# Kernel tuning notes

Hardware: AMD Instinct MI355X
Metric: run time of the kernel (lower is better)

Reference implementation:

```python
import jax, jax.numpy as jnp
import numpy as np
import math

T, S, B, E, H = 2048, 2048, 4, 1024, 16
D = E // H


def setup_inputs() -> dict:
    key = jax.random.key(0)
    ks = jax.random.split(key, 12)
    inp = {
        "query": jax.random.normal(ks[0], (T, B, E), jnp.float32),
        "key": jax.random.normal(ks[1], (S, B, E), jnp.float32),
        "value": jax.random.normal(ks[2], (S, B, E), jnp.float32),
        # causal mask: True means masked (matches torch masked_fill semantics)
        "attn_mask": jnp.triu(jnp.ones((T, S), dtype=bool), k=1),
        # torch Linear layout: weight [out_features, in_features]
        "Wq": jax.random.normal(ks[3], (E, E), jnp.float32) * (1.0 / math.sqrt(E)),
        "bq": jax.random.normal(ks[4], (E,), jnp.float32) * 0.02,
        "Wk": jax.random.normal(ks[5], (E, E), jnp.float32) * (1.0 / math.sqrt(E)),
        "bk": jax.random.normal(ks[6], (E,), jnp.float32) * 0.02,
        "Wv": jax.random.normal(ks[7], (E, E), jnp.float32) * (1.0 / math.sqrt(E)),
        "bv": jax.random.normal(ks[8], (E,), jnp.float32) * 0.02,
        "Wo": jax.random.normal(ks[9], (E, E), jnp.float32) * (1.0 / math.sqrt(E)),
        "bo": jax.random.normal(ks[10], (E,), jnp.float32) * 0.02,
    }
    return inp


def reference(query, key, value, attn_mask, Wq, bq, Wk, bk, Wv, bv, Wo, bo):
    # inputs are [T/S, B, E] (batch_first=False); compute in [B, H, T, D]
    q = (jnp.einsum('tbe,fe->btf', query, Wq) + bq).reshape(B, T, H, D).transpose(0, 2, 1, 3)
    k = (jnp.einsum('sbe,fe->bsf', key, Wk) + bk).reshape(B, S, H, D).transpose(0, 2, 1, 3)
    v = (jnp.einsum('sbe,fe->bsf', value, Wv) + bv).reshape(B, S, H, D).transpose(0, 2, 1, 3)

    scores = jnp.einsum('bhtd,bhsd->bhts', q, k) / math.sqrt(D)  # [B,H,T,S]
    masked = jnp.where(attn_mask[None, None, :, :], -jnp.inf, scores)
    # custom numerics: epsilon-shifted softmax, then re-zero -inf positions
    probs = jax.nn.softmax(masked + 1e-9, axis=-1)
    probs = jnp.where(jnp.isinf(masked), 0.0, probs)

    out = jnp.einsum('bhts,bhsd->bhtd', probs, v)  # [B,H,T,D]
    out = out.transpose(0, 2, 1, 3).reshape(B, T, E)
    out = out @ Wo.T + bo
    return out.transpose(1, 0, 2)  # back to [T, B, E]
```

## Files before the change

kernel.cpp:

```cpp
#include <hip/hip_runtime.h>

typedef unsigned short u16;
typedef __attribute__((ext_vector_type(8))) __bf16 bf16x8;
typedef __attribute__((ext_vector_type(4))) float f32x4;
typedef __attribute__((ext_vector_type(16))) float f32x16;
typedef __attribute__((ext_vector_type(4))) unsigned short u16x4;
typedef __attribute__((ext_vector_type(8))) unsigned short u16x8;
typedef __attribute__((ext_vector_type(4))) unsigned int u32x4;

#define T_LEN 2048
#define B_SZ 4
#define E_DIM 1024
#define H_N 16
#define D_H 64
#define M_ROWS (T_LEN * B_SZ)
#define NQT (T_LEN / 128)

__device__ __forceinline__ u16 f2bf(float f){
  unsigned u = __builtin_bit_cast(unsigned, f);
  u += 0x7fffu + ((u >> 16) & 1u);
  return (u16)(u >> 16);
}

__device__ __forceinline__ float fexp2(float x){
#if __has_builtin(__builtin_amdgcn_exp2f)
  return __builtin_amdgcn_exp2f(x);
#else
  return exp2f(x);
#endif
}

__device__ __forceinline__ unsigned cvtpk(float lo, float hi){
  unsigned w;
  asm("v_cvt_pk_bf16_f32 %0, %1, %2" : "=v"(w) : "v"(lo), "v"(hi));
  return w;
}
__device__ __forceinline__ float xhalf_max(float x){
  return fmaxf(x, __shfl_xor(x, 32));
}
__device__ __forceinline__ float xhalf_sum(float x){
  return x + __shfl_xor(x, 32);
}

__device__ __forceinline__ void load_lds16(const void* g, void* l){
  __builtin_amdgcn_global_load_lds(
      (const __attribute__((address_space(1))) void*)g,
      (__attribute__((address_space(3))) void*)l, 16, 0, 0);
}

__global__ void cvt_all(
    const float* __restrict__ i0, const float* __restrict__ i1, const float* __restrict__ i2,
    const float* __restrict__ i3, const float* __restrict__ i4, const float* __restrict__ i5,
    const float* __restrict__ i6,
    u16* __restrict__ o0, u16* __restrict__ o1, u16* __restrict__ o2,
    u16* __restrict__ o3, u16* __restrict__ o4, u16* __restrict__ o5,
    u16* __restrict__ o6, int nX, int nW)
{
  const int z = blockIdx.z;
  const float* in; u16* out; int n;
  switch (z){
    case 0: in=i0; out=o0; n=nX; break;
    case 1: in=i1; out=o1; n=nX; break;
    case 2: in=i2; out=o2; n=nX; break;
    case 3: in=i3; out=o3; n=nW; break;
    case 4: in=i4; out=o4; n=nW; break;
    case 5: in=i5; out=o5; n=nW; break;
    default: in=i6; out=o6; n=nW; break;
  }
  int idx = (blockIdx.x * blockDim.x + threadIdx.x) * 4;
  int stride = gridDim.x * blockDim.x * 4;
  for (int i = idx; i < n; i += stride){
    float4 v = *(const float4*)(in + i);
    u16x4 o = { f2bf(v.x), f2bf(v.y), f2bf(v.z), f2bf(v.w) };
    *(u16x4*)(out + i) = o;
  }
}

#define G4_LDSU16 32768

__device__ __forceinline__ void stageG(const u16* __restrict__ G, int r0g, int k0,
                                       char* base, int buf, int tid){
  #pragma unroll
  for (int r=0;r<2;++r){
    int c = r*256 + tid;
    int row = c >> 2;
    int colb = ((c & 3) * 16) ^ (((row >> 2) & 3) << 4);
    load_lds16((const char*)(G + (size_t)(r0g + row)*E_DIM + k0) + colb,
               base + buf*8192 + (size_t)(r*256 + (tid >> 6)*64)*16);
  }
}

__device__ __forceinline__ void gemm4_mainloop(
    const u16* __restrict__ A, const u16* __restrict__ Bt,
    int m0, int n0, u16* smem, f32x4 (&acc)[4][4])
{
  constexpr int NT = E_DIM / 32;
  const int tid = threadIdx.x;
  const int lane = tid & 63;
  const int w = tid >> 6;
  const int wr = w >> 1, wc = w & 1;
  const int lr = lane & 15, lg = lane >> 4;
  char* Abase = (char*)smem;
  char* Bbase = (char*)smem + 32768;

  #pragma unroll
  for (int i=0;i<4;i++)
    #pragma unroll
    for (int j=0;j<4;j++) acc[i][j] = (f32x4){0.f,0.f,0.f,0.f};

  stageG(A,  m0, 0,  Abase, 0, tid);
  stageG(Bt, n0, 0,  Bbase, 0, tid);
  stageG(A,  m0, 32, Abase, 1, tid);
  stageG(Bt, n0, 32, Bbase, 1, tid);
  asm volatile("s_waitcnt vmcnt(4)\n" ::: "memory");
  __builtin_amdgcn_sched_barrier(0);
  __builtin_amdgcn_s_barrier();

  const int cbx = (lg*16) ^ (((lr >> 2) & 3) << 4);

  for (int t = 0; t < NT; ++t){
    const int buf = t & 3;
    if (t + 2 < NT){
      stageG(A,  m0, (t+2)*32, Abase, (t+2) & 3, tid);
      stageG(Bt, n0, (t+2)*32, Bbase, (t+2) & 3, tid);
    }
    char* Ac = Abase + buf*8192;
    char* Bc = Bbase + buf*8192;
    bf16x8 af[4], bfr[4];
    #pragma unroll
    for (int i=0;i<4;i++){
      af[i]  = *(const bf16x8*)(Ac + (wr*64 + i*16 + lr)*64 + cbx);
      bfr[i] = *(const bf16x8*)(Bc + (wc*64 + i*16 + lr)*64 + cbx);
    }
    asm volatile("s_waitcnt lgkmcnt(0)\n" ::: "memory");
    __builtin_amdgcn_sched_barrier(0);
    __builtin_amdgcn_s_setprio(1);
    #pragma unroll
    for (int i=0;i<4;i++)
      #pragma unroll
      for (int j=0;j<4;j++)
        acc[i][j] = __builtin_amdgcn_mfma_f32_16x16x32_bf16(af[i], bfr[j], acc[i][j], 0,0,0);
    __builtin_amdgcn_s_setprio(0);
    if (t + 2 < NT)      asm volatile("s_waitcnt vmcnt(4)\n" ::: "memory");
    else if (t + 1 < NT) asm volatile("s_waitcnt vmcnt(0)\n" ::: "memory");
    __builtin_amdgcn_sched_barrier(0);
    __builtin_amdgcn_s_barrier();
  }
}

__device__ __forceinline__ void xcd_remap_gemm(int &m0, int &n0){
  int L = blockIdx.y * 8 + blockIdx.x;
  int c = L & 7, i = L >> 3;
  int by = c*8 + (i & 7);
  int bx = i >> 3;
  m0 = by * 128; n0 = bx * 128;
}

struct QKVArgs {
  const u16* A[3]; const u16* Bw[3]; const float* bias[3];
  float scale[3]; u16* out[3];
};

__global__ __launch_bounds__(256) void gemm_qkv(QKVArgs args){
  __shared__ __align__(16) u16 smem[G4_LDSU16];
  const int z = blockIdx.z;
  int m0, n0; xcd_remap_gemm(m0, n0);
  f32x4 acc[4][4];
  gemm4_mainloop(args.A[z], args.Bw[z], m0, n0, smem, acc);

  const int lane = threadIdx.x & 63;
  const int w = threadIdx.x >> 6;
  const int wr = w >> 1, wc = w & 1;
  const int lr = lane & 15, lg = lane >> 4;
  const float* bias = args.bias[z];
  const float scale = args.scale[z];
  u16* outB = args.out[z];
  #pragma unroll
  for (int i=0;i<4;i++)
    #pragma unroll
    for (int j=0;j<4;j++)
      #pragma unroll
      for (int q=0;q<4;q++){
        int m = m0 + wr*64 + i*16 + lg*4 + q;
        int n = n0 + wc*64 + j*16 + lr;
        float v = (acc[i][j][q] + bias[n]) * scale;
        int t = m >> 2, b = m & 3;
        int h = n >> 6, d = n & 63;
        outB[ ((size_t)(b*H_N + h)*T_LEN + t)*D_H + d ] = f2bf(v);
      }
}

__global__ __launch_bounds__(256) void gemm_out(
    const u16* __restrict__ A, const u16* __restrict__ Bt,
    const float* __restrict__ bias, float* __restrict__ outF)
{
  __shared__ __align__(16) u16 smem[G4_LDSU16];
  int m0, n0; xcd_remap_gemm(m0, n0);
  f32x4 acc[4][4];
  gemm4_mainloop(A, Bt, m0, n0, smem, acc);

  const int lane = threadIdx.x & 63;
  const int w = threadIdx.x >> 6;
  const int wr = w >> 1, wc = w & 1;
  const int lr = lane & 15, lg = lane >> 4;
  #pragma unroll
  for (int i=0;i<4;i++)
    #pragma unroll
    for (int j=0;j<4;j++)
      #pragma unroll
      for (int q=0;q<4;q++){
        int m = m0 + wr*64 + i*16 + lg*4 + q;
        int n = n0 + wc*64 + j*16 + lr;
        float v = acc[i][j][q] + bias[n];
        int b = m >> 11, t = m & 2047;
        outF[ (size_t)(t*B_SZ + b)*E_DIM + n ] = v;
      }
}

__global__ __launch_bounds__(256) void transpose_v(const u16* __restrict__ Vb, u16* __restrict__ Vt){
  __shared__ u16 tile[64][65];
  int bh = blockIdx.y, s0 = blockIdx.x * 64;
  const u16* src = Vb + ((size_t)bh*T_LEN + s0)*D_H;
  u16* dst = Vt + (size_t)bh*D_H*T_LEN + s0;
  int tid = threadIdx.x;
  #pragma unroll
  for (int r=0;r<2;++r){
    int c = r*256 + tid;
    int s = c >> 3, d0 = (c & 7)*8;
    u16x8 v = *(const u16x8*)(src + (size_t)s*D_H + d0);
    #pragma unroll
    for (int j=0;j<8;j++) tile[d0+j][s] = v[j];
  }
  __syncthreads();
  #pragma unroll
  for (int r=0;r<2;++r){
    int c = r*256 + tid;
    int d = c >> 3, s1 = (c & 7)*8;
    u16x8 v;
    #pragma unroll
    for (int j=0;j<8;j++){
      int p = s1 + j;
      int sp = (p & ~12) | ((p & 4) << 1) | ((p & 8) >> 1);
      v[j] = tile[d][sp];
    }
    *(u16x8*)(dst + (size_t)d*T_LEN + s1) = v;
  }
}

__global__ __launch_bounds__(256) void attn_fwd(
    const u16* __restrict__ Qb, const u16* __restrict__ Kb,
    const u16* __restrict__ Vt, u16* __restrict__ AO)
{
  __shared__ __align__(16) u16 smem[4*64*64];
  u16* Ks = smem;
  u16* Vs = smem + 2*64*64;
  const int tid = threadIdx.x;
  const int lane = tid & 63;
  const int wq = tid >> 6;
  const int l31 = lane & 31;
  const int hi = lane >> 5;
  int bh, px;
  {
    int L = blockIdx.y * 8 + blockIdx.x;
    int c = L & 7, i2 = L >> 3;
    bh = c*8 + (i2 & 7);
    px = i2 >> 3;
  }
  const u16* Kbase = Kb + (size_t)bh * T_LEN * D_H;
  const u16* Vbase = Vt + (size_t)bh * D_H * T_LEN;
  const int b_ = bh >> 4, h = bh & 15;

  auto STAGE = [&](int j, int b){
    int s0 = j * 64;
    #pragma unroll
    for (int r=0;r<2;++r){
      int c = r*256 + tid;
      int row = c >> 3;
      int colb = (c & 7) * 16;
      int scolb = colb ^ ((row & 7) << 4);
      load_lds16((const char*)(Kbase + (size_t)(s0 + row)*D_H) + scolb,
                 (char*)Ks + b*8192 + (r*256 + wq*64)*16);
      load_lds16((const char*)(Vbase + (size_t)row*T_LEN + s0) + scolb,
                 (char*)Vs + b*8192 + (r*256 + wq*64)*16);
    }
  };

  #pragma unroll 1
  for (int ph = 0; ph < 2; ++ph){
    const int qt = ph ? px : (NQT - 1 - px);
    const int qb = qt * 128;
    const int qg = qb + wq*32 + l31;

    bf16x8 qf[4];
    {
      const u16* qp = Qb + (size_t)bh*T_LEN*D_H + (size_t)qg*D_H + hi*8;
      #pragma unroll
      for (int kk=0;kk<4;++kk) qf[kk] = *(const bf16x8*)(qp + kk*16);
    }

    f32x16 o[2];
    #pragma unroll
    for (int f=0;f<2;++f)
      #pragma unroll
      for (int r=0;r<16;++r) o[f][r] = 0.f;
    float m_run = -INFINITY, l_run = 0.f;

    const int ntiles = 2*qt + 2;
    __syncthreads();
    STAGE(0, 0);
    __syncthreads();

    for (int j = 0; j < ntiles; ++j){
      const int cur = j & 1;
      if (j + 1 < ntiles) STAGE(j+1, cur^1);
      const char* Kc = (const char*)Ks + cur*8192;
      const char* Vc = (const char*)Vs + cur*8192;

      const bool fullmask = (j == 2*qt + 1) && (wq < 2);
      if (!fullmask){
        f32x16 st[2];
        #pragma unroll
        for (int i=0;i<2;++i)
          #pragma unroll
          for (int r=0;r<16;++r) st[i][r] = 0.f;
        __builtin_amdgcn_s_setprio(1);
        #pragma unroll
        for (int i=0;i<2;++i){
          #pragma unroll
          for (int kk=0;kk<4;++kk){
            int row = i*32 + l31;
            int colb = (kk*32 + hi*16) ^ ((row & 7) << 4);
            bf16x8 kf = *(const bf16x8*)(Kc + row*128 + colb);
            st[i] = __builtin_amdgcn_mfma_f32_32x32x16_bf16(kf, qf[kk], st[i], 0,0,0);
          }
        }
        __builtin_amdgcn_s_setprio(0);

        const int s0 = j*64;
        float mx = -INFINITY;
        if (j >= 2*qt){
          #pragma unroll
          for (int i=0;i<2;++i)
            #pragma unroll
            for (int r=0;r<16;++r){
              int sg = s0 + i*32 + (r&3) + 8*(r>>2) + 4*hi;
              float v = (sg > qg) ? -INFINITY : st[i][r];
              st[i][r] = v;
              mx = fmaxf(mx, v);
            }
        } else {
          #pragma unroll
          for (int i=0;i<2;++i)
            #pragma unroll
            for (int r=0;r<16;++r) mx = fmaxf(mx, st[i][r]);
        }
        mx = xhalf_max(mx);

        if (!__all(mx <= m_run + 8.0f)){
          float m_new = fmaxf(m_run, mx);
          float sc = fexp2(m_run - m_new);
          l_run *= sc;
          #pragma unroll
          for (int f=0;f<2;++f)
            #pragma unroll
            for (int r=0;r<16;++r) o[f][r] *= sc;
          m_run = m_new;
        }

        float rsum = 0.f;
        #pragma unroll
        for (int i=0;i<2;++i)
          #pragma unroll
          for (int r=0;r<16;++r){
            float p = fexp2(st[i][r] - m_run);
            st[i][r] = p;
            rsum += p;
          }
        l_run += xhalf_sum(rsum);

        u32x4 Bfr[4];
        #pragma unroll
        for (int i=0;i<2;++i){
          Bfr[2*i]   = (u32x4){ cvtpk(st[i][0],  st[i][1]),  cvtpk(st[i][2],  st[i][3]),
                                cvtpk(st[i][4],  st[i][5]),  cvtpk(st[i][6],  st[i][7]) };
          Bfr[2*i+1] = (u32x4){ cvtpk(st[i][8],  st[i][9]),  cvtpk(st[i][10], st[i][11]),
                                cvtpk(st[i][12], st[i][13]), cvtpk(st[i][14], st[i][15]) };
        }

        __builtin_amdgcn_s_setprio(1);
        #pragma unroll
        for (int ss=0; ss<4; ++ss){
          bf16x8 pb = __builtin_bit_cast(bf16x8, Bfr[ss]);
          #pragma unroll
          for (int f=0; f<2; ++f){
            int row = f*32 + l31;
            int colb = (ss*32 + hi*16) ^ ((row & 7) << 4);
            bf16x8 vf = *(const bf16x8*)(Vc + row*128 + colb);
            o[f] = __builtin_amdgcn_mfma_f32_32x32x16_bf16(vf, pb, o[f], 0,0,0);
          }
        }
        __builtin_amdgcn_s_setprio(0);
      }
      __syncthreads();
    }

    float linv = 1.f / l_run;
    {
      char* Osh = (char*)smem;
      unsigned base = wq*4352;
      #pragma unroll
      for (int f=0;f<2;++f)
        #pragma unroll
        for (int m=0;m<8;++m){
          unsigned word = cvtpk(o[f][2*m]*linv, o[f][2*m+1]*linv);
          int d0 = (m&1)*2 + 8*(m>>1) + 4*hi + 32*f;
          *(unsigned*)(Osh + base + l31*136 + d0*2) = word;
        }
    }
    __syncthreads();
    {
      int q = tid >> 1, half = tid & 1;
      const char* src = (const char*)smem + (q>>5)*4352 + (q&31)*136 + half*64;
      u16* dst = AO + ((size_t)(b_*T_LEN + qb + q))*E_DIM + h*D_H + half*32;
      #pragma unroll
      for (int k=0;k<4;++k)
        *(u16x8*)(dst + k*8) = *(const u16x8*)(src + k*16);
    }
  }
}

extern "C" void kernel_launch(void* const* d_in, const int* in_sizes, int n_in,
                              void* d_out, int out_size, void* d_ws, size_t ws_size,
                              hipStream_t stream){
  const float* query = (const float*)d_in[0];
  const float* key   = (const float*)d_in[1];
  const float* value = (const float*)d_in[2];
  const float* Wq = (const float*)d_in[4];
  const float* bq = (const float*)d_in[5];
  const float* Wk = (const float*)d_in[6];
  const float* bk = (const float*)d_in[7];
  const float* Wv = (const float*)d_in[8];
  const float* bv = (const float*)d_in[9];
  const float* Wo = (const float*)d_in[10];
  const float* bo = (const float*)d_in[11];

  char* ws = (char*)d_ws;
  const size_t SZ_X = (size_t)M_ROWS * E_DIM * 2;
  const size_t SZ_W = (size_t)E_DIM * E_DIM * 2;
  u16* Xq  = (u16*)(ws);
  u16* Xk  = (u16*)(ws + SZ_X);
  u16* Xv  = (u16*)(ws + 2*SZ_X);
  u16* Wqb = (u16*)(ws + 3*SZ_X);
  u16* Wkb = (u16*)(ws + 3*SZ_X + 1*SZ_W);
  u16* Wvb = (u16*)(ws + 3*SZ_X + 2*SZ_W);
  u16* Wob = (u16*)(ws + 3*SZ_X + 3*SZ_W);
  u16* Qb  = (u16*)(ws + 3*SZ_X + 4*SZ_W);
  u16* Kb  = (u16*)(ws + 4*SZ_X + 4*SZ_W);
  u16* Vb  = (u16*)(ws + 5*SZ_X + 4*SZ_W);
  u16* Vt  = Xk;
  u16* AO  = Xq;

  const int nX = M_ROWS * E_DIM;
  const int nW = E_DIM * E_DIM;
  cvt_all<<<dim3(1024,1,7), 256, 0, stream>>>(
      query, key, value, Wq, Wk, Wv, Wo,
      Xq, Xk, Xv, Wqb, Wkb, Wvb, Wob, nX, nW);

  const float QSCALE = 0.125f * 1.44269504f;
  QKVArgs qa;
  qa.A[0]=Xq;  qa.A[1]=Xk;  qa.A[2]=Xv;
  qa.Bw[0]=Wqb; qa.Bw[1]=Wkb; qa.Bw[2]=Wvb;
  qa.bias[0]=bq; qa.bias[1]=bk; qa.bias[2]=bv;
  qa.scale[0]=QSCALE; qa.scale[1]=1.0f; qa.scale[2]=1.0f;
  qa.out[0]=Qb; qa.out[1]=Kb; qa.out[2]=Vb;
  gemm_qkv<<<dim3(8, M_ROWS/128, 3), 256, 0, stream>>>(qa);
  transpose_v<<<dim3(T_LEN/64, B_SZ*H_N), 256, 0, stream>>>(Vb, Vt);
  attn_fwd<<<dim3(NQT/2, B_SZ*H_N), 256, 0, stream>>>(Qb, Kb, Vt, AO);
  gemm_out<<<dim3(8, M_ROWS/128), 256, 0, stream>>>(AO, Wob, bo, (float*)d_out);
}
```

Before: 180.7 us.

## Shrink attention blocks to 64 query rows and compute row sums via MFMA

The attention kernel now uses 128-thread blocks covering 64 query rows, launched on twice as many blocks. This removes the fully-masked half-tile idle waves and gives finer causal load balancing. The softmax row sum is now accumulated with an extra MFMA against a ones vector instead of scalar adds and a cross-lane shuffle. In exchange, each loaded K/V tile is reused by fewer waves, so LDS staging traffic per query rises, and the extra MFMA adds matrix work per tile.

```diff
diff --git a/kernel.cpp b/kernel.cpp
--- a/kernel.cpp
+++ b/kernel.cpp
@@ -14,7 +14,7 @@
 #define H_N 16
 #define D_H 64
 #define M_ROWS (T_LEN * B_SZ)
-#define NQT (T_LEN / 128)
+#define NQT64 (T_LEN / 64)
 
 __device__ __forceinline__ u16 f2bf(float f){
   unsigned u = __builtin_bit_cast(unsigned, f);
@@ -38,8 +38,16 @@
 __device__ __forceinline__ float xhalf_max(float x){
   return fmaxf(x, __shfl_xor(x, 32));
 }
-__device__ __forceinline__ float xhalf_sum(float x){
-  return x + __shfl_xor(x, 32);
+__device__ __forceinline__ float vmax16(const f32x16 &v){
+  float m = fmaxf(v[0], v[1]);
+  m = fmaxf(fmaxf(m, v[2]),  v[3]);
+  m = fmaxf(fmaxf(m, v[4]),  v[5]);
+  m = fmaxf(fmaxf(m, v[6]),  v[7]);
+  m = fmaxf(fmaxf(m, v[8]),  v[9]);
+  m = fmaxf(fmaxf(m, v[10]), v[11]);
+  m = fmaxf(fmaxf(m, v[12]), v[13]);
+  m = fmaxf(fmaxf(m, v[14]), v[15]);
+  return m;
 }
 
 __device__ __forceinline__ void load_lds16(const void* g, void* l){
@@ -247,7 +255,7 @@
   }
 }
 
-__global__ __launch_bounds__(256) void attn_fwd(
+__global__ __launch_bounds__(128) void attn_fwd(
     const u16* __restrict__ Qb, const u16* __restrict__ Kb,
     const u16* __restrict__ Vt, u16* __restrict__ AO)
 {
@@ -261,7 +269,7 @@
   const int hi = lane >> 5;
   int bh, px;
   {
-    int L = blockIdx.y * 8 + blockIdx.x;
+    int L = blockIdx.y * 16 + blockIdx.x;
     int c = L & 7, i2 = L >> 3;
     bh = c*8 + (i2 & 7);
     px = i2 >> 3;
@@ -270,25 +278,28 @@
   const u16* Vbase = Vt + (size_t)bh * D_H * T_LEN;
   const int b_ = bh >> 4, h = bh & 15;
 
+  const u32x4 onesw = {0x3F803F80u, 0x3F803F80u, 0x3F803F80u, 0x3F803F80u};
+  const bf16x8 onesf = __builtin_bit_cast(bf16x8, onesw);
+
   auto STAGE = [&](int j, int b){
     int s0 = j * 64;
     #pragma unroll
-    for (int r=0;r<2;++r){
-      int c = r*256 + tid;
+    for (int r=0;r<4;++r){
+      int c = r*128 + tid;
       int row = c >> 3;
       int colb = (c & 7) * 16;
       int scolb = colb ^ ((row & 7) << 4);
       load_lds16((const char*)(Kbase + (size_t)(s0 + row)*D_H) + scolb,
-                 (char*)Ks + b*8192 + (r*256 + wq*64)*16);
+                 (char*)Ks + b*8192 + (size_t)c*16);
       load_lds16((const char*)(Vbase + (size_t)row*T_LEN + s0) + scolb,
-                 (char*)Vs + b*8192 + (r*256 + wq*64)*16);
+                 (char*)Vs + b*8192 + (size_t)c*16);
     }
   };
 
   #pragma unroll 1
   for (int ph = 0; ph < 2; ++ph){
-    const int qt = ph ? px : (NQT - 1 - px);
-    const int qb = qt * 128;
+    const int qt = ph ? px : (NQT64 - 1 - px);
+    const int qb = qt * 64;
     const int qg = qb + wq*32 + l31;
 
     bf16x8 qf[4];
@@ -298,14 +309,16 @@
       for (int kk=0;kk<4;++kk) qf[kk] = *(const bf16x8*)(qp + kk*16);
     }
 
-    f32x16 o[2];
+    f32x16 o[2], sumacc;
     #pragma unroll
     for (int f=0;f<2;++f)
       #pragma unroll
       for (int r=0;r<16;++r) o[f][r] = 0.f;
-    float m_run = -INFINITY, l_run = 0.f;
-
-    const int ntiles = 2*qt + 2;
+    #pragma unroll
+    for (int r=0;r<16;++r) sumacc[r] = 0.f;
+    float m_run = -INFINITY;
+
+    const int ntiles = qt + 1;
     __syncthreads();
     STAGE(0, 0);
     __syncthreads();
@@ -316,31 +329,31 @@
       const char* Kc = (const char*)Ks + cur*8192;
       const char* Vc = (const char*)Vs + cur*8192;
 
-      const bool fullmask = (j == 2*qt + 1) && (wq < 2);
-      if (!fullmask){
-        f32x16 st[2];
-        #pragma unroll
-        for (int i=0;i<2;++i)
-          #pragma unroll
-          for (int r=0;r<16;++r) st[i][r] = 0.f;
-        __builtin_amdgcn_s_setprio(1);
+      f32x16 st[2];
+      #pragma unroll
+      for (int i=0;i<2;++i)
+        #pragma unroll
+        for (int r=0;r<16;++r) st[i][r] = 0.f;
+      __builtin_amdgcn_s_setprio(1);
+      #pragma unroll
+      for (int i=0;i<2;++i){
+        #pragma unroll
+        for (int kk=0;kk<4;++kk){
+          int row = i*32 + l31;
+          int colb = (kk*32 + hi*16) ^ ((row & 7) << 4);
+          bf16x8 kf = *(const bf16x8*)(Kc + row*128 + colb);
+          st[i] = __builtin_amdgcn_mfma_f32_32x32x16_bf16(kf, qf[kk], st[i], 0,0,0);
+        }
+      }
+      __builtin_amdgcn_s_setprio(0);
+
+      const bool diag = (j == qt);
+      const int s0 = j*64;
+      float mx = -INFINITY;
+      if (diag){
         #pragma unroll
         for (int i=0;i<2;++i){
-          #pragma unroll
-          for (int kk=0;kk<4;++kk){
-            int row = i*32 + l31;
-            int colb = (kk*32 + hi*16) ^ ((row & 7) << 4);
-            bf16x8 kf = *(const bf16x8*)(Kc + row*128 + colb);
-            st[i] = __builtin_amdgcn_mfma_f32_32x32x16_bf16(kf, qf[kk], st[i], 0,0,0);
-          }
-        }
-        __builtin_amdgcn_s_setprio(0);
-
-        const int s0 = j*64;
-        float mx = -INFINITY;
-        if (j >= 2*qt){
-          #pragma unroll
-          for (int i=0;i<2;++i)
+          if (i >= wq){
             #pragma unroll
             for (int r=0;r<16;++r){
               int sg = s0 + i*32 + (r&3) + 8*(r>>2) + 4*hi;
@@ -348,63 +361,58 @@
               st[i][r] = v;
               mx = fmaxf(mx, v);
             }
-        } else {
-          #pragma unroll
-          for (int i=0;i<2;++i)
-            #pragma unroll
-            for (int r=0;r<16;++r) mx = fmaxf(mx, st[i][r]);
-        }
-        mx = xhalf_max(mx);
-
-        if (!__all(mx <= m_run + 8.0f)){
-          float m_new = fmaxf(m_run, mx);
-          float sc = fexp2(m_run - m_new);
-          l_run *= sc;
-          #pragma unroll
-          for (int f=0;f<2;++f)
-            #pragma unroll
-            for (int r=0;r<16;++r) o[f][r] *= sc;
-          m_run = m_new;
-        }
-
-        float rsum = 0.f;
-        #pragma unroll
-        for (int i=0;i<2;++i)
-          #pragma unroll
-          for (int r=0;r<16;++r){
-            float p = fexp2(st[i][r] - m_run);
-            st[i][r] = p;
-            rsum += p;
-          }
-        l_run += xhalf_sum(rsum);
-
-        u32x4 Bfr[4];
-        #pragma unroll
-        for (int i=0;i<2;++i){
-          Bfr[2*i]   = (u32x4){ cvtpk(st[i][0],  st[i][1]),  cvtpk(st[i][2],  st[i][3]),
-                                cvtpk(st[i][4],  st[i][5]),  cvtpk(st[i][6],  st[i][7]) };
-          Bfr[2*i+1] = (u32x4){ cvtpk(st[i][8],  st[i][9]),  cvtpk(st[i][10], st[i][11]),
-                                cvtpk(st[i][12], st[i][13]), cvtpk(st[i][14], st[i][15]) };
-        }
-
-        __builtin_amdgcn_s_setprio(1);
-        #pragma unroll
-        for (int ss=0; ss<4; ++ss){
-          bf16x8 pb = __builtin_bit_cast(bf16x8, Bfr[ss]);
-          #pragma unroll
-          for (int f=0; f<2; ++f){
-            int row = f*32 + l31;
-            int colb = (ss*32 + hi*16) ^ ((row & 7) << 4);
-            bf16x8 vf = *(const bf16x8*)(Vc + row*128 + colb);
-            o[f] = __builtin_amdgcn_mfma_f32_32x32x16_bf16(vf, pb, o[f], 0,0,0);
+          } else {
+            mx = fmaxf(mx, vmax16(st[i]));
           }
         }
-        __builtin_amdgcn_s_setprio(0);
-      }
+      } else {
+        mx = fmaxf(vmax16(st[0]), vmax16(st[1]));
+      }
+      mx = xhalf_max(mx);
+
+      if (!__all(mx <= m_run + 8.0f)){
+        float m_new = fmaxf(m_run, mx);
+        float sc = fexp2(m_run - m_new);
+        sumacc[0] *= sc;
+        #pragma unroll
+        for (int f=0;f<2;++f)
+          #pragma unroll
+          for (int r=0;r<16;++r) o[f][r] *= sc;
+        m_run = m_new;
+      }
+
+      #pragma unroll
+      for (int i=0;i<2;++i)
+        #pragma unroll
+        for (int r=0;r<16;++r) st[i][r] = fexp2(st[i][r] - m_run);
+
+      u32x4 Bfr[4];
+      #pragma unroll
+      for (int i=0;i<2;++i){
+        Bfr[2*i]   = (u32x4){ cvtpk(st[i][0],  st[i][1]),  cvtpk(st[i][2],  st[i][3]),
+                              cvtpk(st[i][4],  st[i][5]),  cvtpk(st[i][6],  st[i][7]) };
+        Bfr[2*i+1] = (u32x4){ cvtpk(st[i][8],  st[i][9]),  cvtpk(st[i][10], st[i][11]),
+                              cvtpk(st[i][12], st[i][13]), cvtpk(st[i][14], st[i][15]) };
+      }
+
+      __builtin_amdgcn_s_setprio(1);
+      #pragma unroll
+      for (int ss=0; ss<4; ++ss){
+        bf16x8 pb = __builtin_bit_cast(bf16x8, Bfr[ss]);
+        #pragma unroll
+        for (int f=0; f<2; ++f){
+          int row = f*32 + l31;
+          int colb = (ss*32 + hi*16) ^ ((row & 7) << 4);
+          bf16x8 vf = *(const bf16x8*)(Vc + row*128 + colb);
+          o[f] = __builtin_amdgcn_mfma_f32_32x32x16_bf16(vf, pb, o[f], 0,0,0);
+        }
+        sumacc = __builtin_amdgcn_mfma_f32_32x32x16_bf16(onesf, pb, sumacc, 0,0,0);
+      }
+      __builtin_amdgcn_s_setprio(0);
       __syncthreads();
     }
 
-    float linv = 1.f / l_run;
+    float linv = 1.f / sumacc[0];
     {
       char* Osh = (char*)smem;
       unsigned base = wq*4352;
@@ -475,6 +483,6 @@
   qa.out[0]=Qb; qa.out[1]=Kb; qa.out[2]=Vb;
   gemm_qkv<<<dim3(8, M_ROWS/128, 3), 256, 0, stream>>>(qa);
   transpose_v<<<dim3(T_LEN/64, B_SZ*H_N), 256, 0, stream>>>(Vb, Vt);
-  attn_fwd<<<dim3(NQT/2, B_SZ*H_N), 256, 0, stream>>>(Qb, Kb, Vt, AO);
+  attn_fwd<<<dim3(16, B_SZ*H_N), 128, 0, stream>>>(Qb, Kb, Vt, AO);
   gemm_out<<<dim3(8, M_ROWS/128), 256, 0, stream>>>(AO, Wob, bo, (float*)d_out);
 }
```

Result: slower. 203.9 us (+12.9%).
